# Performance work log

Measured on AMD Instinct MI355X. Metric: run time of the kernel, lower is better.

## Reference

```python
import jax, jax.numpy as jnp
import numpy as np

B, T, DIN, E, H, P = 8, 2048, 256, 256, 4, 8
HD = E // H


def _xavier(key, out_dim, in_dim):
    lim = float(np.sqrt(6.0 / (in_dim + out_dim)))
    return jax.random.uniform(key, (out_dim, in_dim), jnp.float32, -lim, lim)


def setup_inputs() -> dict:
    key = jax.random.key(0)
    ks = jax.random.split(key, 9)
    return {
        "x": jax.random.normal(ks[0], (B, T, DIN), jnp.float32),
        "w_in": _xavier(ks[1], E, DIN), "b_in": jnp.zeros((E,), jnp.float32),
        # MHA in-projections (torch packs qkv; xavier over packed [3E,E] approximated per-slice)
        "w_q": _xavier(ks[2], E, E), "b_q": jnp.zeros((E,), jnp.float32),
        "w_k": _xavier(ks[3], E, E), "b_k": jnp.zeros((E,), jnp.float32),
        "w_v": _xavier(ks[4], E, E), "b_v": jnp.zeros((E,), jnp.float32),
        "w_o": _xavier(ks[5], E, E), "b_o": jnp.zeros((E,), jnp.float32),
        "w_bd": _xavier(ks[6], 1, E), "b_bd": jnp.zeros((1,), jnp.float32),
        "w_pr": _xavier(ks[7], E, E), "b_pr": jnp.zeros((E,), jnp.float32),
    }


def reference(x, w_in, b_in, w_q, b_q, w_k, b_k, w_v, b_v, w_o, b_o, w_bd, b_bd, w_pr, b_pr):
    b, t, _ = x.shape
    h = x @ w_in.T + b_in                                   # [B,T,E]
    # self-attention (batch_first MHA, eval mode -> dropout is identity)
    q = (h @ w_q.T + b_q).reshape(b, t, H, HD)
    k = (h @ w_k.T + b_k).reshape(b, t, H, HD)
    v = (h @ w_v.T + b_v).reshape(b, t, H, HD)
    scale = 1.0 / np.sqrt(HD).astype(np.float32)
    scores = jnp.einsum("bqhd,bkhd->bhqk", q * scale, k)   # [B,H,T,T]
    attn = jax.nn.softmax(scores, axis=-1)
    ao = jnp.einsum("bhqk,bkhd->bqhd", attn, v).reshape(b, t, E)
    ao = ao @ w_o.T + b_o
    # boundary scoring -> dynamic patch ids
    bs = jax.nn.sigmoid(ao @ w_bd.T + b_bd)[..., 0]         # [B,T]
    cum = jnp.cumsum(bs, axis=1)
    normalized = cum / jnp.maximum(cum[:, -1:], 1e-6)
    pid = jnp.minimum((normalized * P).astype(jnp.int32), P - 1)  # [B,T]
    # mean-pool h into P dynamic patches (scatter_add + counts, via one-hot segment matmul)
    oh = jax.nn.one_hot(pid, P, dtype=h.dtype)              # [B,T,P]
    patch_emb = jnp.einsum("btp,btd->bpd", oh, h)           # [B,P,E]
    counts = oh.sum(axis=1)[..., None]                      # [B,P,1]
    patch_emb = patch_emb / jnp.maximum(counts, 1.0)
    return patch_emb @ w_pr.T + b_pr                        # [B,P,E]
```

## Files before the change

### kernel.cpp

```cpp
#include <hip/hip_runtime.h>
#include <cstddef>

#define NB 8
#define NT 2048
#define NE 256
#define NH 4
#define ND 64
#define NP 8

typedef short bf16x8 __attribute__((ext_vector_type(8)));
typedef float f32x4 __attribute__((ext_vector_type(4)));

__device__ __forceinline__ unsigned short f2bf(float f) {
  unsigned u = __builtin_bit_cast(unsigned, f);
  u += 0x7fffu + ((u >> 16) & 1u);
  return (unsigned short)(u >> 16);
}
__device__ __forceinline__ float bf2f(unsigned short h) {
  unsigned u = ((unsigned)h) << 16;
  return __builtin_bit_cast(float, u);
}
__device__ __forceinline__ void split2(float a, float b, unsigned& hi, unsigned& lo) {
  const unsigned short ha = f2bf(a), hb = f2bf(b);
  hi = (unsigned)ha | ((unsigned)hb << 16);
  const unsigned short la = f2bf(a - bf2f(ha));
  const unsigned short lb = f2bf(b - bf2f(hb));
  lo = (unsigned)la | ((unsigned)lb << 16);
}
__device__ __forceinline__ void gld16(const void* g, void* l) {
  __builtin_amdgcn_global_load_lds((const __attribute__((address_space(1))) unsigned*)g,
                                   (__attribute__((address_space(3))) unsigned*)l, 16, 0, 0);
}

#define QSC 0.180336880111120419f

__global__ __launch_bounds__(256) void setup_kernel(
    const float* __restrict__ w_in, const float* __restrict__ w_q,
    const float* __restrict__ w_k, const float* __restrict__ b_q,
    const float* __restrict__ b_k, const float* __restrict__ w_o,
    const float* __restrict__ b_o, const float* __restrict__ w_bd,
    const float* __restrict__ b_bd, const float* __restrict__ w_v,
    const float* __restrict__ b_v,
    unsigned short* __restrict__ wihi, unsigned short* __restrict__ wilo,
    unsigned short* __restrict__ wqkvhi, unsigned short* __restrict__ wqkvlo,
    float* __restrict__ bqk, float* __restrict__ consts, float* __restrict__ psum)
{
  __shared__ float wbd_s[NE];
  __shared__ float u_s[NE];
  const int b = blockIdx.x, tid = threadIdx.x;
  if (b < 512) {
    const int i = b * 256 + tid;
    const float v = (i < 65536) ? w_q[i] * QSC : w_k[i - 65536];
    const unsigned short h = f2bf(v);
    wqkvhi[i] = h;
    wqkvlo[i] = f2bf(v - bf2f(h));
    if (i < 512) bqk[i] = (i < 256) ? b_q[i] * QSC : b_k[i - 256];
  } else if (b < 576) {
    const int i = (b - 512) * 256 + tid;
    const float4 v = *(const float4*)(w_in + (size_t)i * 4);
    const float vv[4] = {v.x, v.y, v.z, v.w};
    unsigned short h4[4], l4[4];
    #pragma unroll
    for (int j = 0; j < 4; ++j) {
      h4[j] = f2bf(vv[j]);
      l4[j] = f2bf(vv[j] - bf2f(h4[j]));
    }
    *(ushort2*)(wihi + (size_t)i * 4)     = make_ushort2(h4[0], h4[1]);
    *(ushort2*)(wihi + (size_t)i * 4 + 2) = make_ushort2(h4[2], h4[3]);
    *(ushort2*)(wilo + (size_t)i * 4)     = make_ushort2(l4[0], l4[1]);
    *(ushort2*)(wilo + (size_t)i * 4 + 2) = make_ushort2(l4[2], l4[3]);
  } else if (b == 576) {
    wbd_s[tid] = w_bd[tid];
    __syncthreads();
    float a = 0.f;
    for (int j = 0; j < NE; ++j) a = fmaf(wbd_s[j], w_o[j * NE + tid], a);
    u_s[tid] = a;
    __syncthreads();
    #pragma unroll
    for (int hh = 0; hh < NH; ++hh) {
      float a2 = 0.f;
      for (int d = 0; d < ND; ++d)
        a2 = fmaf(u_s[hh * ND + d], w_v[(size_t)(hh * ND + d) * NE + tid], a2);
      const unsigned short hb = f2bf(a2);
      wqkvhi[(512 + hh) * 256 + tid] = hb;
      wqkvlo[(512 + hh) * 256 + tid] = f2bf(a2 - bf2f(hb));
    }
    for (int i = tid; i < 60 * 256; i += 256) {
      wqkvhi[516 * 256 + i] = 0;
      wqkvlo[516 * 256 + i] = 0;
    }
    if (tid == 0) {
      float cc = 0.f;
      for (int j = 0; j < NE; ++j) cc = fmaf(wbd_s[j], b_o[j], cc);
      consts[0] = cc + b_bd[0];
    }
    if (tid < 4) {
      float cv = 0.f;
      for (int d = 0; d < ND; ++d) cv = fmaf(u_s[tid * ND + d], b_v[tid * ND + d], cv);
      bqk[512 + tid] = cv;
    } else if (tid < 64) {
      bqk[512 + tid] = 0.f;
    }
  } else {
    for (int i = tid; i < NB * NP * NE; i += 256) psum[i] = 0.f;
  }
}

__global__ __launch_bounds__(256) void hgemm_kernel(
    const float* __restrict__ x,
    const unsigned short* __restrict__ wihi, const unsigned short* __restrict__ wilo,
    const float* __restrict__ b_in,
    unsigned short* __restrict__ hhi, unsigned short* __restrict__ hlo)
{
  __shared__ __align__(16) char sm[2][24576];
  const int tid = threadIdx.x;
  const int wave = tid >> 6, lane = tid & 63;
  const int lr = lane & 15, lg = lane >> 4;
  const int wm = wave >> 1, wn = wave & 1;
  const int bid = blockIdx.x;
  const int idx = bid >> 3;
  const int m0 = ((bid & 7) * 16 + (idx >> 2)) * 128;
  const int n0 = (idx & 3) * 64;

  const float* aSrc[4];
  #pragma unroll
  for (int c = 0; c < 4; ++c) {
    const int L = c * 4096 + tid * 16;
    const int row = L >> 7, w = (L >> 4) & 7;
    aSrc[c] = x + (size_t)(m0 + row) * 256 + (w ^ (row & 7)) * 4;
  }
  const unsigned short* wSrc[2];
  #pragma unroll
  for (int c = 0; c < 2; ++c) {
    const int L = c * 4096 + tid * 16;
    const int half = (L >> 12) & 1;
    const int Lh = L & 4095;
    const int col = Lh >> 6, w = (Lh >> 4) & 3;
    wSrc[c] = (half ? wilo : wihi) + (size_t)(n0 + col) * 256 + (w ^ ((col >> 1) & 3)) * 8;
  }
  int aoff[4][2], woff[2];
  #pragma unroll
  for (int s = 0; s < 4; ++s) {
    const int row = wm * 64 + s * 16 + lr;
    const int b0 = row * 128 + lg * 32;
    const int f = (row & 7) << 4;
    aoff[s][0] = b0 ^ f;
    aoff[s][1] = (b0 + 16) ^ f;
  }
  #pragma unroll
  for (int ns = 0; ns < 2; ++ns) {
    const int col = wn * 32 + ns * 16 + lr;
    woff[ns] = (col * 64 + lg * 16) ^ (((col >> 1) & 3) << 4);
  }

  f32x4 acc[4][2];
  #pragma unroll
  for (int s = 0; s < 4; ++s)
    #pragma unroll
    for (int ns = 0; ns < 2; ++ns) acc[s][ns] = (f32x4){0.f, 0.f, 0.f, 0.f};

  {
    char* lb = sm[0];
    #pragma unroll
    for (int c = 0; c < 4; ++c) gld16(aSrc[c], lb + c * 4096 + wave * 1024);
    #pragma unroll
    for (int c = 0; c < 2; ++c) gld16(wSrc[c], lb + 16384 + c * 4096 + wave * 1024);
  }

  for (int kt = 0; kt < 8; ++kt) {
    __syncthreads();
    if (kt < 7) {
      char* nb = sm[(kt + 1) & 1];
      #pragma unroll
      for (int c = 0; c < 4; ++c) gld16(aSrc[c] + (kt + 1) * 32, nb + c * 4096 + wave * 1024);
      #pragma unroll
      for (int c = 0; c < 2; ++c) gld16(wSrc[c] + (kt + 1) * 32, nb + 16384 + c * 4096 + wave * 1024);
    }
    const char* lb = sm[kt & 1];
    bf16x8 ah[4], al[4], wh[2], wl[2];
    #pragma unroll
    for (int s = 0; s < 4; ++s) {
      const f32x4 p0 = *(const f32x4*)(lb + aoff[s][0]);
      const f32x4 p1 = *(const f32x4*)(lb + aoff[s][1]);
      unsigned h0, h1, h2, h3, l0, l1, l2, l3;
      split2(p0[0], p0[1], h0, l0);
      split2(p0[2], p0[3], h1, l1);
      split2(p1[0], p1[1], h2, l2);
      split2(p1[2], p1[3], h3, l3);
      const uint4 hu = make_uint4(h0, h1, h2, h3);
      const uint4 lu = make_uint4(l0, l1, l2, l3);
      ah[s] = __builtin_bit_cast(bf16x8, hu);
      al[s] = __builtin_bit_cast(bf16x8, lu);
    }
    #pragma unroll
    for (int ns = 0; ns < 2; ++ns) {
      wh[ns] = *(const bf16x8*)(lb + 16384 + woff[ns]);
      wl[ns] = *(const bf16x8*)(lb + 20480 + woff[ns]);
    }
    #pragma unroll
    for (int s = 0; s < 4; ++s)
      #pragma unroll
      for (int ns = 0; ns < 2; ++ns) {
        acc[s][ns] = __builtin_amdgcn_mfma_f32_16x16x32_bf16(ah[s], wh[ns], acc[s][ns], 0, 0, 0);
        acc[s][ns] = __builtin_amdgcn_mfma_f32_16x16x32_bf16(ah[s], wl[ns], acc[s][ns], 0, 0, 0);
        acc[s][ns] = __builtin_amdgcn_mfma_f32_16x16x32_bf16(al[s], wh[ns], acc[s][ns], 0, 0, 0);
      }
  }
  #pragma unroll
  for (int s = 0; s < 4; ++s)
    #pragma unroll
    for (int ns = 0; ns < 2; ++ns)
      #pragma unroll
      for (int reg = 0; reg < 4; ++reg) {
        const int row = m0 + wm * 64 + s * 16 + lg * 4 + reg;
        const int col = n0 + wn * 32 + ns * 16 + lr;
        const float v = acc[s][ns][reg] + b_in[col];
        const size_t i2 = (size_t)row * 256 + col;
        const unsigned short hb = f2bf(v);
        hhi[i2] = hb;
        hlo[i2] = f2bf(v - bf2f(hb));
      }
}

__global__ __launch_bounds__(256) void qkvgemm_kernel(
    const unsigned short* __restrict__ Ahi, const unsigned short* __restrict__ Alo,
    const unsigned short* __restrict__ Whi, const unsigned short* __restrict__ Wlo,
    const float* __restrict__ bias,
    unsigned short* __restrict__ Qhi, unsigned short* __restrict__ Qlo,
    unsigned short* __restrict__ Khi, unsigned short* __restrict__ Klo,
    float* __restrict__ vubuf)
{
  __shared__ __align__(16) char sm[2][24576];
  const int tid = threadIdx.x;
  const int wave = tid >> 6, lane = tid & 63;
  const int lr = lane & 15, lg = lane >> 4;
  const int wm = wave >> 1, wn = wave & 1;
  const int bid = blockIdx.x;
  const int idx = bid >> 3;
  const int m0 = ((bid & 7) * 16 + idx / 9) * 128;
  const int n0 = (idx % 9) * 64;

  const unsigned short* aSrc[4];
  #pragma unroll
  for (int c = 0; c < 4; ++c) {
    const int L = c * 4096 + tid * 16;
    const int half = L >> 13;
    const int Lh = L & 8191;
    const int row = Lh >> 6, w = (Lh >> 4) & 3;
    aSrc[c] = (half ? Alo : Ahi) + (size_t)(m0 + row) * 256 + (w ^ ((row >> 1) & 3)) * 8;
  }
  const unsigned short* wSrc[2];
  #pragma unroll
  for (int c = 0; c < 2; ++c) {
    const int L = c * 4096 + tid * 16;
    const int half = (L >> 12) & 1;
    const int Lh = L & 4095;
    const int col = Lh >> 6, w = (Lh >> 4) & 3;
    wSrc[c] = (half ? Wlo : Whi) + (size_t)(n0 + col) * 256 + (w ^ ((col >> 1) & 3)) * 8;
  }
  int aoff[4], woff[2];
  #pragma unroll
  for (int s = 0; s < 4; ++s) {
    const int row = wm * 64 + s * 16 + lr;
    aoff[s] = (row * 64 + lg * 16) ^ (((row >> 1) & 3) << 4);
  }
  #pragma unroll
  for (int ns = 0; ns < 2; ++ns) {
    const int col = wn * 32 + ns * 16 + lr;
    woff[ns] = (col * 64 + lg * 16) ^ (((col >> 1) & 3) << 4);
  }

  f32x4 acc[4][2];
  #pragma unroll
  for (int s = 0; s < 4; ++s)
    #pragma unroll
    for (int ns = 0; ns < 2; ++ns) acc[s][ns] = (f32x4){0.f, 0.f, 0.f, 0.f};

  {
    char* lb = sm[0];
    #pragma unroll
    for (int c = 0; c < 4; ++c) gld16(aSrc[c], lb + c * 4096 + wave * 1024);
    #pragma unroll
    for (int c = 0; c < 2; ++c) gld16(wSrc[c], lb + 16384 + c * 4096 + wave * 1024);
  }

  for (int kt = 0; kt < 8; ++kt) {
    __syncthreads();
    if (kt < 7) {
      char* nb = sm[(kt + 1) & 1];
      #pragma unroll
      for (int c = 0; c < 4; ++c) gld16(aSrc[c] + (kt + 1) * 32, nb + c * 4096 + wave * 1024);
      #pragma unroll
      for (int c = 0; c < 2; ++c) gld16(wSrc[c] + (kt + 1) * 32, nb + 16384 + c * 4096 + wave * 1024);
    }
    const char* lb = sm[kt & 1];
    bf16x8 ah[4], al[4], wh[2], wl[2];
    #pragma unroll
    for (int s = 0; s < 4; ++s) {
      ah[s] = *(const bf16x8*)(lb + aoff[s]);
      al[s] = *(const bf16x8*)(lb + 8192 + aoff[s]);
    }
    #pragma unroll
    for (int ns = 0; ns < 2; ++ns) {
      wh[ns] = *(const bf16x8*)(lb + 16384 + woff[ns]);
      wl[ns] = *(const bf16x8*)(lb + 20480 + woff[ns]);
    }
    #pragma unroll
    for (int s = 0; s < 4; ++s)
      #pragma unroll
      for (int ns = 0; ns < 2; ++ns) {
        acc[s][ns] = __builtin_amdgcn_mfma_f32_16x16x32_bf16(ah[s], wh[ns], acc[s][ns], 0, 0, 0);
        acc[s][ns] = __builtin_amdgcn_mfma_f32_16x16x32_bf16(ah[s], wl[ns], acc[s][ns], 0, 0, 0);
        acc[s][ns] = __builtin_amdgcn_mfma_f32_16x16x32_bf16(al[s], wh[ns], acc[s][ns], 0, 0, 0);
      }
  }
  #pragma unroll
  for (int s = 0; s < 4; ++s)
    #pragma unroll
    for (int ns = 0; ns < 2; ++ns)
      #pragma unroll
      for (int reg = 0; reg < 4; ++reg) {
        const int row = m0 + wm * 64 + s * 16 + lg * 4 + reg;
        const int col = n0 + wn * 32 + ns * 16 + lr;
        const float v = acc[s][ns][reg] + bias[col];
        const int b = row >> 11, t = row & 2047;
        if (col < 512) {
          const int c = col & 255;
          const int head = c >> 6, d = c & 63;
          const size_t i2 = (((size_t)(b * NH + head)) * NT + t) * ND + d;
          const unsigned short hb = f2bf(v);
          if (col < 256) { Qhi[i2] = hb; Qlo[i2] = f2bf(v - bf2f(hb)); }
          else           { Khi[i2] = hb; Klo[i2] = f2bf(v - bf2f(hb)); }
        } else if (col < 516) {
          vubuf[((size_t)(b * NH + (col - 512))) * NT + t] = v;
        }
      }
}

__global__ __launch_bounds__(512) void attn_kernel8(
    const unsigned short* __restrict__ qhi, const unsigned short* __restrict__ qlo,
    const unsigned short* __restrict__ khi, const unsigned short* __restrict__ klo,
    const float* __restrict__ vu, float2* __restrict__ part2)
{
  __shared__ __align__(16) char kbuf[4][16384];
  __shared__ float vu_s[256];
  const int tid = threadIdx.x;
  const int wave = tid >> 6, lane = tid & 63;
  const int lr = lane & 15, lg = lane >> 4;
  const int bid = blockIdx.x;
  const int idx = bid >> 3;
  const int bh = (bid & 7) * 4 + (idx >> 6);
  const int rem = idx & 63;
  const int qt = rem >> 3, kh = rem & 7;
  const size_t base = (size_t)bh * NT * ND;
  const int qrow0 = qt * 256 + wave * 32;
  const int krow0 = kh * 256;

  if (tid < 256) vu_s[tid] = vu[(size_t)bh * NT + krow0 + tid];

  bf16x8 qf[2][2][2];
  #pragma unroll
  for (int s = 0; s < 2; ++s)
    #pragma unroll
    for (int ds = 0; ds < 2; ++ds) {
      const size_t off = base + (size_t)(qrow0 + s * 16 + lr) * ND + ds * 32 + lg * 8;
      qf[s][ds][0] = *(const bf16x8*)(qhi + off);
      qf[s][ds][1] = *(const bf16x8*)(qlo + off);
    }

  const int so = (tid * 16) ^ (((tid >> 3) & 7) << 4);
  int ro0[4], ro1[4];
  #pragma unroll
  for (int ns = 0; ns < 4; ++ns) {
    const int r = ns * 16 + lr;
    const int sw = (r & 7) << 4;
    const int ob = r * 128 + lg * 16;
    ro0[ns] = ob ^ sw;
    ro1[ns] = (ob + 64) ^ sw;
  }
  const char* srcH = (const char*)(khi + base + (size_t)krow0 * ND);
  const char* srcL = (const char*)(klo + base + (size_t)krow0 * ND);
  #pragma unroll
  for (int t = 0; t < 4; ++t) {
    gld16(srcH + t * 8192 + so, &kbuf[t][wave * 1024]);
    gld16(srcL + t * 8192 + so, &kbuf[t][8192 + wave * 1024]);
  }
  __syncthreads();

  float l[8], sv[8];
  #pragma unroll
  for (int i = 0; i < 8; ++i) { l[i] = 0.f; sv[i] = 0.f; }
  const f32x4 Z = (f32x4){0.f, 0.f, 0.f, 0.f};

  #pragma unroll
  for (int it = 0; it < 4; ++it) {
    const int kt = (it + wave) & 3;
    const char* kb = (const char*)kbuf[kt];
    f32x4 acc[2][4];
    float vuv[4];
    __builtin_amdgcn_s_setprio(1);
    #pragma unroll
    for (int ns = 0; ns < 4; ++ns) {
      const bf16x8 kh0 = *(const bf16x8*)(kb + ro0[ns]);
      const bf16x8 kh1 = *(const bf16x8*)(kb + ro1[ns]);
      const bf16x8 kl0 = *(const bf16x8*)(kb + 8192 + ro0[ns]);
      const bf16x8 kl1 = *(const bf16x8*)(kb + 8192 + ro1[ns]);
      vuv[ns] = vu_s[kt * 64 + ns * 16 + lr];
      #pragma unroll
      for (int s = 0; s < 2; ++s) {
        acc[s][ns] = __builtin_amdgcn_mfma_f32_16x16x32_bf16(qf[s][0][0], kh0, Z, 0, 0, 0);
        acc[s][ns] = __builtin_amdgcn_mfma_f32_16x16x32_bf16(qf[s][0][0], kl0, acc[s][ns], 0, 0, 0);
        acc[s][ns] = __builtin_amdgcn_mfma_f32_16x16x32_bf16(qf[s][0][1], kh0, acc[s][ns], 0, 0, 0);
        acc[s][ns] = __builtin_amdgcn_mfma_f32_16x16x32_bf16(qf[s][1][0], kh1, acc[s][ns], 0, 0, 0);
        acc[s][ns] = __builtin_amdgcn_mfma_f32_16x16x32_bf16(qf[s][1][0], kl1, acc[s][ns], 0, 0, 0);
        acc[s][ns] = __builtin_amdgcn_mfma_f32_16x16x32_bf16(qf[s][1][1], kh1, acc[s][ns], 0, 0, 0);
      }
    }
    __builtin_amdgcn_s_setprio(0);
    #pragma unroll
    for (int s = 0; s < 2; ++s)
      #pragma unroll
      for (int reg = 0; reg < 4; ++reg) {
        const int ri = s * 4 + reg;
        #pragma unroll
        for (int ns = 0; ns < 4; ++ns) {
          const float e = __builtin_amdgcn_exp2f(acc[s][ns][reg]);
          l[ri] += e;
          sv[ri] = fmaf(e, vuv[ns], sv[ri]);
        }
      }
  }
  #pragma unroll
  for (int ri = 0; ri < 8; ++ri) {
    #pragma unroll
    for (int off = 1; off < 16; off <<= 1) {
      l[ri]  += __shfl_xor(l[ri],  off, 16);
      sv[ri] += __shfl_xor(sv[ri], off, 16);
    }
  }
  if (lr == 0) {
    #pragma unroll
    for (int s = 0; s < 2; ++s)
      #pragma unroll
      for (int reg = 0; reg < 4; ++reg) {
        const int row = qrow0 + s * 16 + lg * 4 + reg;
        part2[(((size_t)bh * NT + row) << 3) + kh] = make_float2(l[s * 4 + reg], sv[s * 4 + reg]);
      }
  }
}

__global__ __launch_bounds__(256) void combine_kernel(
    const float4* __restrict__ part4, const float* __restrict__ consts,
    float* __restrict__ bs)
{
  const int gid = blockIdx.x * 256 + threadIdx.x;
  const int b = gid >> 11, t = gid & 2047;
  float logit = consts[0];
  #pragma unroll
  for (int hh = 0; hh < NH; ++hh) {
    const size_t p0 = ((size_t)((b * NH + hh) * NT) + t) * 4;
    float lsum = 0.f, ssum = 0.f;
    #pragma unroll
    for (int q = 0; q < 4; ++q) {
      const float4 p = part4[p0 + q];
      lsum += p.x + p.z;
      ssum += p.y + p.w;
    }
    logit += ssum / lsum;
  }
  bs[gid] = 1.f / (1.f + expf(-logit));
}

__global__ __launch_bounds__(256) void boundary_kernel(
    const float* __restrict__ bs, int* __restrict__ pid, int* __restrict__ counts)
{
  const int b = blockIdx.x, tid = threadIdx.x;
  __shared__ float partial[256];
  __shared__ int cnt_s[8];
  float v[8];
  float run = 0.f;
  const float4 b0 = *(const float4*)(bs + b * NT + tid * 8);
  const float4 b1 = *(const float4*)(bs + b * NT + tid * 8 + 4);
  const float bv[8] = {b0.x, b0.y, b0.z, b0.w, b1.x, b1.y, b1.z, b1.w};
  #pragma unroll
  for (int i = 0; i < 8; ++i) { run += bv[i]; v[i] = run; }
  float x = run;
  partial[tid] = x;
  __syncthreads();
  for (int off = 1; off < 256; off <<= 1) {
    const float y = (tid >= off) ? partial[tid - off] : 0.f;
    __syncthreads();
    x += y;
    partial[tid] = x;
    __syncthreads();
  }
  const float total = partial[255];
  if (tid < 8) cnt_s[tid] = 0;
  __syncthreads();
  const float denom = fmaxf(total, 1e-6f);
  const float excl = x - run;
  #pragma unroll
  for (int i = 0; i < 8; ++i) {
    const float norm = (excl + v[i]) / denom;
    int pp = (int)(norm * 8.f);
    pp = pp > 7 ? 7 : pp;
    pid[b * NT + tid * 8 + i] = pp;
    atomicAdd(&cnt_s[pp], 1);
  }
  __syncthreads();
  if (tid < 8) counts[b * 8 + tid] = cnt_s[tid];
}

__global__ __launch_bounds__(256) void pool_kernel(
    const unsigned short* __restrict__ hhi, const int* __restrict__ pid,
    float* __restrict__ psum)
{
  const int b = blockIdx.x >> 4, chunk = blockIdx.x & 15;
  const int tid = threadIdx.x;
  __shared__ int pid_s[128];
  const int t0 = chunk * 128;
  if (tid < 128) pid_s[tid] = pid[b * NT + t0 + tid];
  __syncthreads();
  float acc[8] = {};
  for (int tok = 0; tok < 128; ++tok) {
    const float val = bf2f(hhi[((size_t)b * NT + t0 + tok) * NE + tid]);
    const int p = pid_s[tok];
    #pragma unroll
    for (int pp = 0; pp < 8; ++pp) acc[pp] += (p == pp) ? val : 0.f;
  }
  #pragma unroll
  for (int pp = 0; pp < 8; ++pp)
    atomicAdd(&psum[((size_t)b * NP + pp) * NE + tid], acc[pp]);
}

__global__ __launch_bounds__(256) void final_kernel(
    const float* __restrict__ psum, const int* __restrict__ counts,
    const float* __restrict__ w_pr, const float* __restrict__ b_pr, float* __restrict__ out)
{
  const int bp = blockIdx.x;
  const int tid = threadIdx.x;
  __shared__ float pe[NE];
  const float cnt = fmaxf((float)counts[bp], 1.f);
  pe[tid] = psum[(size_t)bp * NE + tid] / cnt;
  __syncthreads();
  float acc = 0.f;
  for (int e = 0; e < NE; ++e) acc = fmaf(pe[e], w_pr[(size_t)tid * NE + e], acc);
  out[(size_t)bp * NE + tid] = acc + b_pr[tid];
}

extern "C" void kernel_launch(void* const* d_in, const int* in_sizes, int n_in,
                              void* d_out, int out_size, void* d_ws, size_t ws_size,
                              hipStream_t stream) {
  (void)in_sizes; (void)n_in; (void)out_size; (void)ws_size;
  const float* x    = (const float*)d_in[0];
  const float* w_in = (const float*)d_in[1];
  const float* b_in = (const float*)d_in[2];
  const float* w_q  = (const float*)d_in[3];
  const float* b_q  = (const float*)d_in[4];
  const float* w_k  = (const float*)d_in[5];
  const float* b_k  = (const float*)d_in[6];
  const float* w_v  = (const float*)d_in[7];
  const float* b_v  = (const float*)d_in[8];
  const float* w_o  = (const float*)d_in[9];
  const float* b_o  = (const float*)d_in[10];
  const float* w_bd = (const float*)d_in[11];
  const float* b_bd = (const float*)d_in[12];
  const float* w_pr = (const float*)d_in[13];
  const float* b_pr = (const float*)d_in[14];
  float* out = (float*)d_out;

  const size_t M = (size_t)NB * NT;
  unsigned short* hhi = (unsigned short*)d_ws;
  unsigned short* hlo = hhi + M * NE;
  unsigned short* qhi = hlo + M * NE;
  unsigned short* qlo = qhi + M * NE;
  unsigned short* khi = qlo + M * NE;
  unsigned short* klo = khi + M * NE;
  unsigned short* wihi = klo + M * NE;
  unsigned short* wilo = wihi + 65536;
  unsigned short* wqkvhi = wilo + 65536;
  unsigned short* wqkvlo = wqkvhi + 147456;
  float* bqk    = (float*)(wqkvlo + 147456);
  float* vubuf  = bqk + 576;
  float* part   = vubuf + 65536;
  float* bsbuf  = part + 1048576;
  float* consts = bsbuf + 16384;
  float* psum   = consts + 8;
  int*   pid    = (int*)(psum + 16384);
  int*   counts = pid + 16384;

  setup_kernel<<<578, 256, 0, stream>>>(w_in, w_q, w_k, b_q, b_k, w_o, b_o,
      w_bd, b_bd, w_v, b_v, wihi, wilo, wqkvhi, wqkvlo, bqk, consts, psum);
  hgemm_kernel<<<512, 256, 0, stream>>>(x, wihi, wilo, b_in, hhi, hlo);
  qkvgemm_kernel<<<1152, 256, 0, stream>>>(hhi, hlo, wqkvhi, wqkvlo, bqk,
      qhi, qlo, khi, klo, vubuf);
  attn_kernel8<<<2048, 512, 0, stream>>>(qhi, qlo, khi, klo, vubuf, (float2*)part);
  combine_kernel<<<64, 256, 0, stream>>>((const float4*)part, consts, bsbuf);
  boundary_kernel<<<8, 256, 0, stream>>>(bsbuf, pid, counts);
  pool_kernel<<<128, 256, 0, stream>>>(hhi, pid, psum);
  final_kernel<<<64, 256, 0, stream>>>(psum, counts, w_pr, b_pr, out);
}
```

Baseline: 154.1 us.

## Fold input projection into QKV weights and switch attention to 32x32 MFMA

Weights are precomposed on the device (w_q·w_in, w_k·w_in, and the v/boundary vector·w_in, with their biases folded in), so a single GEMM from x produces h, Q, K and the V-projection scalars. This removes the separate h GEMM pass and the hi/lo h round trip through memory. The attention kernel moves from 16x16x32 to 32x32x16 MFMA tiles with 16-row accumulators and adds an occupancy hint to launch bounds. The cost is an extra small setup kernel, a larger fused GEMM grid, and changed rounding from composing the weights before the bf16 split.

```diff
diff --git a/kernel.cpp b/kernel.cpp
--- a/kernel.cpp
+++ b/kernel.cpp
@@ -10,6 +10,7 @@
 
 typedef short bf16x8 __attribute__((ext_vector_type(8)));
 typedef float f32x4 __attribute__((ext_vector_type(4)));
+typedef float f32x16 __attribute__((ext_vector_type(16)));
 
 __device__ __forceinline__ unsigned short f2bf(float f) {
   unsigned u = __builtin_bit_cast(unsigned, f);
@@ -34,83 +35,93 @@
 
 #define QSC 0.180336880111120419f
 
-__global__ __launch_bounds__(256) void setup_kernel(
-    const float* __restrict__ w_in, const float* __restrict__ w_q,
-    const float* __restrict__ w_k, const float* __restrict__ b_q,
-    const float* __restrict__ b_k, const float* __restrict__ w_o,
-    const float* __restrict__ b_o, const float* __restrict__ w_bd,
-    const float* __restrict__ b_bd, const float* __restrict__ w_v,
-    const float* __restrict__ b_v,
-    unsigned short* __restrict__ wihi, unsigned short* __restrict__ wilo,
-    unsigned short* __restrict__ wqkvhi, unsigned short* __restrict__ wqkvlo,
-    float* __restrict__ bqk, float* __restrict__ consts, float* __restrict__ psum)
+__global__ __launch_bounds__(256) void setup1_kernel(
+    const float* __restrict__ w_o, const float* __restrict__ b_o,
+    const float* __restrict__ w_bd, const float* __restrict__ b_bd,
+    const float* __restrict__ w_v, const float* __restrict__ b_v,
+    float* __restrict__ uvbuf, float* __restrict__ consts)
 {
   __shared__ float wbd_s[NE];
   __shared__ float u_s[NE];
+  const int tid = threadIdx.x;
+  wbd_s[tid] = w_bd[tid];
+  __syncthreads();
+  float a = 0.f;
+  for (int j = 0; j < NE; ++j) a = fmaf(wbd_s[j], w_o[j * NE + tid], a);
+  u_s[tid] = a;
+  __syncthreads();
+  #pragma unroll
+  for (int hh = 0; hh < NH; ++hh) {
+    float a2 = 0.f;
+    for (int d = 0; d < ND; ++d)
+      a2 = fmaf(u_s[hh * ND + d], w_v[(size_t)(hh * ND + d) * NE + tid], a2);
+    uvbuf[hh * NE + tid] = a2;
+  }
+  if (tid == 0) {
+    float cc = 0.f;
+    for (int j = 0; j < NE; ++j) cc = fmaf(wbd_s[j], b_o[j], cc);
+    consts[0] = cc + b_bd[0];
+  }
+  if (tid >= 8 && tid < 12) {
+    const int hh = tid - 8;
+    float cv = 0.f;
+    for (int d = 0; d < ND; ++d) cv = fmaf(u_s[hh * ND + d], b_v[hh * ND + d], cv);
+    consts[1 + hh] = cv;
+  }
+}
+
+__global__ __launch_bounds__(256) void setup2_kernel(
+    const float* __restrict__ w_in, const float* __restrict__ w_q,
+    const float* __restrict__ w_k, const float* __restrict__ b_in,
+    const float* __restrict__ b_q, const float* __restrict__ b_k,
+    const float* __restrict__ uvbuf, const float* __restrict__ consts,
+    unsigned short* __restrict__ wfhi, unsigned short* __restrict__ wflo,
+    float* __restrict__ bias_f, float* __restrict__ psum)
+{
+  __shared__ float row_s[256];
+  __shared__ float red[256];
   const int b = blockIdx.x, tid = threadIdx.x;
-  if (b < 512) {
-    const int i = b * 256 + tid;
-    const float v = (i < 65536) ? w_q[i] * QSC : w_k[i - 65536];
-    const unsigned short h = f2bf(v);
-    wqkvhi[i] = h;
-    wqkvlo[i] = f2bf(v - bf2f(h));
-    if (i < 512) bqk[i] = (i < 256) ? b_q[i] * QSC : b_k[i - 256];
-  } else if (b < 576) {
-    const int i = (b - 512) * 256 + tid;
-    const float4 v = *(const float4*)(w_in + (size_t)i * 4);
-    const float vv[4] = {v.x, v.y, v.z, v.w};
-    unsigned short h4[4], l4[4];
-    #pragma unroll
-    for (int j = 0; j < 4; ++j) {
-      h4[j] = f2bf(vv[j]);
-      l4[j] = f2bf(vv[j] - bf2f(h4[j]));
-    }
-    *(ushort2*)(wihi + (size_t)i * 4)     = make_ushort2(h4[0], h4[1]);
-    *(ushort2*)(wihi + (size_t)i * 4 + 2) = make_ushort2(h4[2], h4[3]);
-    *(ushort2*)(wilo + (size_t)i * 4)     = make_ushort2(l4[0], l4[1]);
-    *(ushort2*)(wilo + (size_t)i * 4 + 2) = make_ushort2(l4[2], l4[3]);
-  } else if (b == 576) {
-    wbd_s[tid] = w_bd[tid];
+  if (b == 832) {
+    for (int i = tid; i < NB * NP * NE; i += 256) psum[i] = 0.f;
+    return;
+  }
+  float v = 0.f, bias = 0.f;
+  if (b < 256) {
+    v = w_in[(size_t)b * 256 + tid];
+    bias = b_in[b];
+  } else if (b < 772) {
+    const float* wrow = (b < 512) ? (w_q + (size_t)(b - 256) * 256)
+                      : (b < 768) ? (w_k + (size_t)(b - 512) * 256)
+                                  : (uvbuf + (size_t)(b - 768) * 256);
+    row_s[tid] = wrow[tid];
     __syncthreads();
-    float a = 0.f;
-    for (int j = 0; j < NE; ++j) a = fmaf(wbd_s[j], w_o[j * NE + tid], a);
-    u_s[tid] = a;
+    float acc = 0.f;
+    for (int e = 0; e < 256; ++e) acc = fmaf(row_s[e], w_in[(size_t)e * 256 + tid], acc);
+    v = acc;
+    red[tid] = row_s[tid] * b_in[tid];
     __syncthreads();
-    #pragma unroll
-    for (int hh = 0; hh < NH; ++hh) {
-      float a2 = 0.f;
-      for (int d = 0; d < ND; ++d)
-        a2 = fmaf(u_s[hh * ND + d], w_v[(size_t)(hh * ND + d) * NE + tid], a2);
-      const unsigned short hb = f2bf(a2);
-      wqkvhi[(512 + hh) * 256 + tid] = hb;
-      wqkvlo[(512 + hh) * 256 + tid] = f2bf(a2 - bf2f(hb));
-    }
-    for (int i = tid; i < 60 * 256; i += 256) {
-      wqkvhi[516 * 256 + i] = 0;
-      wqkvlo[516 * 256 + i] = 0;
-    }
-    if (tid == 0) {
-      float cc = 0.f;
-      for (int j = 0; j < NE; ++j) cc = fmaf(wbd_s[j], b_o[j], cc);
-      consts[0] = cc + b_bd[0];
-    }
-    if (tid < 4) {
-      float cv = 0.f;
-      for (int d = 0; d < ND; ++d) cv = fmaf(u_s[tid * ND + d], b_v[tid * ND + d], cv);
-      bqk[512 + tid] = cv;
-    } else if (tid < 64) {
-      bqk[512 + tid] = 0.f;
-    }
-  } else {
-    for (int i = tid; i < NB * NP * NE; i += 256) psum[i] = 0.f;
-  }
-}
-
-__global__ __launch_bounds__(256) void hgemm_kernel(
+    for (int off = 128; off > 0; off >>= 1) {
+      if (tid < off) red[tid] += red[tid + off];
+      __syncthreads();
+    }
+    bias = red[0] + ((b < 512) ? b_q[b - 256] : (b < 768) ? b_k[b - 512]
+                                              : consts[1 + (b - 768)]);
+    if (b < 512) { v *= QSC; bias *= QSC; }
+  }
+  const unsigned short hb = f2bf(v);
+  wfhi[(size_t)b * 256 + tid] = hb;
+  wflo[(size_t)b * 256 + tid] = f2bf(v - bf2f(hb));
+  if (tid == 0) bias_f[b] = bias;
+}
+
+__global__ __launch_bounds__(256) void xgemm_kernel(
     const float* __restrict__ x,
-    const unsigned short* __restrict__ wihi, const unsigned short* __restrict__ wilo,
-    const float* __restrict__ b_in,
-    unsigned short* __restrict__ hhi, unsigned short* __restrict__ hlo)
+    const unsigned short* __restrict__ wfhi, const unsigned short* __restrict__ wflo,
+    const float* __restrict__ bias_f,
+    unsigned short* __restrict__ hhi,
+    unsigned short* __restrict__ Qhi, unsigned short* __restrict__ Qlo,
+    unsigned short* __restrict__ Khi, unsigned short* __restrict__ Klo,
+    float* __restrict__ vubuf)
 {
   __shared__ __align__(16) char sm[2][24576];
   const int tid = threadIdx.x;
@@ -119,8 +130,8 @@
   const int wm = wave >> 1, wn = wave & 1;
   const int bid = blockIdx.x;
   const int idx = bid >> 3;
-  const int m0 = ((bid & 7) * 16 + (idx >> 2)) * 128;
-  const int n0 = (idx & 3) * 64;
+  const int m0 = ((bid & 7) * 16 + idx / 13) * 128;
+  const int n0 = (idx % 13) * 64;
 
   const float* aSrc[4];
   #pragma unroll
@@ -136,7 +147,7 @@
     const int half = (L >> 12) & 1;
     const int Lh = L & 4095;
     const int col = Lh >> 6, w = (Lh >> 4) & 3;
-    wSrc[c] = (half ? wilo : wihi) + (size_t)(n0 + col) * 256 + (w ^ ((col >> 1) & 3)) * 8;
+    wSrc[c] = (half ? wflo : wfhi) + (size_t)(n0 + col) * 256 + (w ^ ((col >> 1) & 3)) * 8;
   }
   int aoff[4][2], woff[2];
   #pragma unroll
@@ -214,130 +225,25 @@
       for (int reg = 0; reg < 4; ++reg) {
         const int row = m0 + wm * 64 + s * 16 + lg * 4 + reg;
         const int col = n0 + wn * 32 + ns * 16 + lr;
-        const float v = acc[s][ns][reg] + b_in[col];
-        const size_t i2 = (size_t)row * 256 + col;
-        const unsigned short hb = f2bf(v);
-        hhi[i2] = hb;
-        hlo[i2] = f2bf(v - bf2f(hb));
-      }
-}
-
-__global__ __launch_bounds__(256) void qkvgemm_kernel(
-    const unsigned short* __restrict__ Ahi, const unsigned short* __restrict__ Alo,
-    const unsigned short* __restrict__ Whi, const unsigned short* __restrict__ Wlo,
-    const float* __restrict__ bias,
-    unsigned short* __restrict__ Qhi, unsigned short* __restrict__ Qlo,
-    unsigned short* __restrict__ Khi, unsigned short* __restrict__ Klo,
-    float* __restrict__ vubuf)
-{
-  __shared__ __align__(16) char sm[2][24576];
-  const int tid = threadIdx.x;
-  const int wave = tid >> 6, lane = tid & 63;
-  const int lr = lane & 15, lg = lane >> 4;
-  const int wm = wave >> 1, wn = wave & 1;
-  const int bid = blockIdx.x;
-  const int idx = bid >> 3;
-  const int m0 = ((bid & 7) * 16 + idx / 9) * 128;
-  const int n0 = (idx % 9) * 64;
-
-  const unsigned short* aSrc[4];
-  #pragma unroll
-  for (int c = 0; c < 4; ++c) {
-    const int L = c * 4096 + tid * 16;
-    const int half = L >> 13;
-    const int Lh = L & 8191;
-    const int row = Lh >> 6, w = (Lh >> 4) & 3;
-    aSrc[c] = (half ? Alo : Ahi) + (size_t)(m0 + row) * 256 + (w ^ ((row >> 1) & 3)) * 8;
-  }
-  const unsigned short* wSrc[2];
-  #pragma unroll
-  for (int c = 0; c < 2; ++c) {
-    const int L = c * 4096 + tid * 16;
-    const int half = (L >> 12) & 1;
-    const int Lh = L & 4095;
-    const int col = Lh >> 6, w = (Lh >> 4) & 3;
-    wSrc[c] = (half ? Wlo : Whi) + (size_t)(n0 + col) * 256 + (w ^ ((col >> 1) & 3)) * 8;
-  }
-  int aoff[4], woff[2];
-  #pragma unroll
-  for (int s = 0; s < 4; ++s) {
-    const int row = wm * 64 + s * 16 + lr;
-    aoff[s] = (row * 64 + lg * 16) ^ (((row >> 1) & 3) << 4);
-  }
-  #pragma unroll
-  for (int ns = 0; ns < 2; ++ns) {
-    const int col = wn * 32 + ns * 16 + lr;
-    woff[ns] = (col * 64 + lg * 16) ^ (((col >> 1) & 3) << 4);
-  }
-
-  f32x4 acc[4][2];
-  #pragma unroll
-  for (int s = 0; s < 4; ++s)
-    #pragma unroll
-    for (int ns = 0; ns < 2; ++ns) acc[s][ns] = (f32x4){0.f, 0.f, 0.f, 0.f};
-
-  {
-    char* lb = sm[0];
-    #pragma unroll
-    for (int c = 0; c < 4; ++c) gld16(aSrc[c], lb + c * 4096 + wave * 1024);
-    #pragma unroll
-    for (int c = 0; c < 2; ++c) gld16(wSrc[c], lb + 16384 + c * 4096 + wave * 1024);
-  }
-
-  for (int kt = 0; kt < 8; ++kt) {
-    __syncthreads();
-    if (kt < 7) {
-      char* nb = sm[(kt + 1) & 1];
-      #pragma unroll
-      for (int c = 0; c < 4; ++c) gld16(aSrc[c] + (kt + 1) * 32, nb + c * 4096 + wave * 1024);
-      #pragma unroll
-      for (int c = 0; c < 2; ++c) gld16(wSrc[c] + (kt + 1) * 32, nb + 16384 + c * 4096 + wave * 1024);
-    }
-    const char* lb = sm[kt & 1];
-    bf16x8 ah[4], al[4], wh[2], wl[2];
-    #pragma unroll
-    for (int s = 0; s < 4; ++s) {
-      ah[s] = *(const bf16x8*)(lb + aoff[s]);
-      al[s] = *(const bf16x8*)(lb + 8192 + aoff[s]);
-    }
-    #pragma unroll
-    for (int ns = 0; ns < 2; ++ns) {
-      wh[ns] = *(const bf16x8*)(lb + 16384 + woff[ns]);
-      wl[ns] = *(const bf16x8*)(lb + 20480 + woff[ns]);
-    }
-    #pragma unroll
-    for (int s = 0; s < 4; ++s)
-      #pragma unroll
-      for (int ns = 0; ns < 2; ++ns) {
-        acc[s][ns] = __builtin_amdgcn_mfma_f32_16x16x32_bf16(ah[s], wh[ns], acc[s][ns], 0, 0, 0);
-        acc[s][ns] = __builtin_amdgcn_mfma_f32_16x16x32_bf16(ah[s], wl[ns], acc[s][ns], 0, 0, 0);
-        acc[s][ns] = __builtin_amdgcn_mfma_f32_16x16x32_bf16(al[s], wh[ns], acc[s][ns], 0, 0, 0);
-      }
-  }
-  #pragma unroll
-  for (int s = 0; s < 4; ++s)
-    #pragma unroll
-    for (int ns = 0; ns < 2; ++ns)
-      #pragma unroll
-      for (int reg = 0; reg < 4; ++reg) {
-        const int row = m0 + wm * 64 + s * 16 + lg * 4 + reg;
-        const int col = n0 + wn * 32 + ns * 16 + lr;
-        const float v = acc[s][ns][reg] + bias[col];
+        const float v = acc[s][ns][reg] + bias_f[col];
         const int b = row >> 11, t = row & 2047;
-        if (col < 512) {
-          const int c = col & 255;
+        if (col < 256) {
+          hhi[(size_t)row * 256 + col] = f2bf(v);
+        } else if (col < 768) {
+          const int c = (col - 256) & 255;
           const int head = c >> 6, d = c & 63;
           const size_t i2 = (((size_t)(b * NH + head)) * NT + t) * ND + d;
           const unsigned short hb = f2bf(v);
-          if (col < 256) { Qhi[i2] = hb; Qlo[i2] = f2bf(v - bf2f(hb)); }
-          else           { Khi[i2] = hb; Klo[i2] = f2bf(v - bf2f(hb)); }
-        } else if (col < 516) {
-          vubuf[((size_t)(b * NH + (col - 512))) * NT + t] = v;
+          const unsigned short lb2 = f2bf(v - bf2f(hb));
+          if (col < 512) { Qhi[i2] = hb; Qlo[i2] = lb2; }
+          else           { Khi[i2] = hb; Klo[i2] = lb2; }
+        } else if (col < 772) {
+          vubuf[((size_t)(b * NH + (col - 768))) * NT + t] = v;
         }
       }
 }
 
-__global__ __launch_bounds__(512) void attn_kernel8(
+__global__ __launch_bounds__(512, 4) void attn_kernel9(
     const unsigned short* __restrict__ qhi, const unsigned short* __restrict__ qlo,
     const unsigned short* __restrict__ khi, const unsigned short* __restrict__ klo,
     const float* __restrict__ vu, float2* __restrict__ part2)
@@ -346,7 +252,8 @@
   __shared__ float vu_s[256];
   const int tid = threadIdx.x;
   const int wave = tid >> 6, lane = tid & 63;
-  const int lr = lane & 15, lg = lane >> 4;
+  const int lk = lane & 31;
+  const int lh = lane >> 5;
   const int bid = blockIdx.x;
   const int idx = bid >> 3;
   const int bh = (bid & 7) * 4 + (idx >> 6);
@@ -358,26 +265,22 @@
 
   if (tid < 256) vu_s[tid] = vu[(size_t)bh * NT + krow0 + tid];
 
-  bf16x8 qf[2][2][2];
-  #pragma unroll
-  for (int s = 0; s < 2; ++s)
-    #pragma unroll
-    for (int ds = 0; ds < 2; ++ds) {
-      const size_t off = base + (size_t)(qrow0 + s * 16 + lr) * ND + ds * 32 + lg * 8;
-      qf[s][ds][0] = *(const bf16x8*)(qhi + off);
-      qf[s][ds][1] = *(const bf16x8*)(qlo + off);
-    }
+  bf16x8 qf[4][2];
+  #pragma unroll
+  for (int ds = 0; ds < 4; ++ds) {
+    const size_t off = base + (size_t)(qrow0 + lk) * ND + ds * 16 + lh * 8;
+    qf[ds][0] = *(const bf16x8*)(qhi + off);
+    qf[ds][1] = *(const bf16x8*)(qlo + off);
+  }
 
   const int so = (tid * 16) ^ (((tid >> 3) & 7) << 4);
-  int ro0[4], ro1[4];
-  #pragma unroll
-  for (int ns = 0; ns < 4; ++ns) {
-    const int r = ns * 16 + lr;
-    const int sw = (r & 7) << 4;
-    const int ob = r * 128 + lg * 16;
-    ro0[ns] = ob ^ sw;
-    ro1[ns] = (ob + 64) ^ sw;
-  }
+  int ro[2][4];
+  #pragma unroll
+  for (int sub = 0; sub < 2; ++sub)
+    #pragma unroll
+    for (int ds = 0; ds < 4; ++ds)
+      ro[sub][ds] = (sub * 32 + lk) * 128 + ((32 * ds + 16 * lh) ^ ((lk & 7) << 4));
+
   const char* srcH = (const char*)(khi + base + (size_t)krow0 * ND);
   const char* srcL = (const char*)(klo + base + (size_t)krow0 * ND);
   #pragma unroll
@@ -387,65 +290,73 @@
   }
   __syncthreads();
 
-  float l[8], sv[8];
-  #pragma unroll
-  for (int i = 0; i < 8; ++i) { l[i] = 0.f; sv[i] = 0.f; }
-  const f32x4 Z = (f32x4){0.f, 0.f, 0.f, 0.f};
+  float l[16], sv[16];
+  #pragma unroll
+  for (int i = 0; i < 16; ++i) { l[i] = 0.f; sv[i] = 0.f; }
+  f32x16 Z;
+  #pragma unroll
+  for (int i = 0; i < 16; ++i) Z[i] = 0.f;
 
   #pragma unroll
   for (int it = 0; it < 4; ++it) {
     const int kt = (it + wave) & 3;
     const char* kb = (const char*)kbuf[kt];
-    f32x4 acc[2][4];
-    float vuv[4];
-    __builtin_amdgcn_s_setprio(1);
-    #pragma unroll
-    for (int ns = 0; ns < 4; ++ns) {
-      const bf16x8 kh0 = *(const bf16x8*)(kb + ro0[ns]);
-      const bf16x8 kh1 = *(const bf16x8*)(kb + ro1[ns]);
-      const bf16x8 kl0 = *(const bf16x8*)(kb + 8192 + ro0[ns]);
-      const bf16x8 kl1 = *(const bf16x8*)(kb + 8192 + ro1[ns]);
-      vuv[ns] = vu_s[kt * 64 + ns * 16 + lr];
+    #pragma unroll
+    for (int sub = 0; sub < 2; ++sub) {
+      const float vuv = vu_s[kt * 64 + sub * 32 + lk];
+      f32x16 acc;
+      __builtin_amdgcn_s_setprio(1);
+      {
+        const bf16x8 kh0 = *(const bf16x8*)(kb + ro[sub][0]);
+        const bf16x8 kl0 = *(const bf16x8*)(kb + 8192 + ro[sub][0]);
+        acc = __builtin_amdgcn_mfma_f32_32x32x16_bf16(qf[0][0], kh0, Z, 0, 0, 0);
+        acc = __builtin_amdgcn_mfma_f32_32x32x16_bf16(qf[0][0], kl0, acc, 0, 0, 0);
+        acc = __builtin_amdgcn_mfma_f32_32x32x16_bf16(qf[0][1], kh0, acc, 0, 0, 0);
+      }
+      {
+        const bf16x8 kh1 = *(const bf16x8*)(kb + ro[sub][1]);
+        const bf16x8 kl1 = *(const bf16x8*)(kb + 8192 + ro[sub][1]);
+        acc = __builtin_amdgcn_mfma_f32_32x32x16_bf16(qf[1][0], kh1, acc, 0, 0, 0);
+        acc = __builtin_amdgcn_mfma_f32_32x32x16_bf16(qf[1][0], kl1, acc, 0, 0, 0);
+        acc = __builtin_amdgcn_mfma_f32_32x32x16_bf16(qf[1][1], kh1, acc, 0, 0, 0);
+      }
+      {
+        const bf16x8 kh2 = *(const bf16x8*)(kb + ro[sub][2]);
+        const bf16x8 kl2 = *(const bf16x8*)(kb + 8192 + ro[sub][2]);
+        acc = __builtin_amdgcn_mfma_f32_32x32x16_bf16(qf[2][0], kh2, acc, 0, 0, 0);
+        acc = __builtin_amdgcn_mfma_f32_32x32x16_bf16(qf[2][0], kl2, acc, 0, 0, 0);
+        acc = __builtin_amdgcn_mfma_f32_32x32x16_bf16(qf[2][1], kh2, acc, 0, 0, 0);
+      }
+      {
+        const bf16x8 kh3 = *(const bf16x8*)(kb + ro[sub][3]);
+        const bf16x8 kl3 = *(const bf16x8*)(kb + 8192 + ro[sub][3]);
+        acc = __builtin_amdgcn_mfma_f32_32x32x16_bf16(qf[3][0], kh3, acc, 0, 0, 0);
+        acc = __builtin_amdgcn_mfma_f32_32x32x16_bf16(qf[3][0], kl3, acc, 0, 0, 0);
+        acc = __builtin_amdgcn_mfma_f32_32x32x16_bf16(qf[3][1], kh3, acc, 0, 0, 0);
+      }
+      __builtin_amdgcn_s_setprio(0);
       #pragma unroll
-      for (int s = 0; s < 2; ++s) {
-        acc[s][ns] = __builtin_amdgcn_mfma_f32_16x16x32_bf16(qf[s][0][0], kh0, Z, 0, 0, 0);
-        acc[s][ns] = __builtin_amdgcn_mfma_f32_16x16x32_bf16(qf[s][0][0], kl0, acc[s][ns], 0, 0, 0);
-        acc[s][ns] = __builtin_amdgcn_mfma_f32_16x16x32_bf16(qf[s][0][1], kh0, acc[s][ns], 0, 0, 0);
-        acc[s][ns] = __builtin_amdgcn_mfma_f32_16x16x32_bf16(qf[s][1][0], kh1, acc[s][ns], 0, 0, 0);
-        acc[s][ns] = __builtin_amdgcn_mfma_f32_16x16x32_bf16(qf[s][1][0], kl1, acc[s][ns], 0, 0, 0);
-        acc[s][ns] = __builtin_amdgcn_mfma_f32_16x16x32_bf16(qf[s][1][1], kh1, acc[s][ns], 0, 0, 0);
-      }
-    }
-    __builtin_amdgcn_s_setprio(0);
-    #pragma unroll
-    for (int s = 0; s < 2; ++s)
-      #pragma unroll
-      for (int reg = 0; reg < 4; ++reg) {
-        const int ri = s * 4 + reg;
-        #pragma unroll
-        for (int ns = 0; ns < 4; ++ns) {
-          const float e = __builtin_amdgcn_exp2f(acc[s][ns][reg]);
-          l[ri] += e;
-          sv[ri] = fmaf(e, vuv[ns], sv[ri]);
-        }
-      }
-  }
-  #pragma unroll
-  for (int ri = 0; ri < 8; ++ri) {
-    #pragma unroll
-    for (int off = 1; off < 16; off <<= 1) {
-      l[ri]  += __shfl_xor(l[ri],  off, 16);
-      sv[ri] += __shfl_xor(sv[ri], off, 16);
-    }
-  }
-  if (lr == 0) {
-    #pragma unroll
-    for (int s = 0; s < 2; ++s)
-      #pragma unroll
-      for (int reg = 0; reg < 4; ++reg) {
-        const int row = qrow0 + s * 16 + lg * 4 + reg;
-        part2[(((size_t)bh * NT + row) << 3) + kh] = make_float2(l[s * 4 + reg], sv[s * 4 + reg]);
-      }
+      for (int reg = 0; reg < 16; ++reg) {
+        const float e = __builtin_amdgcn_exp2f(acc[reg]);
+        l[reg] += e;
+        sv[reg] = fmaf(e, vuv, sv[reg]);
+      }
+    }
+  }
+  #pragma unroll
+  for (int reg = 0; reg < 16; ++reg) {
+    #pragma unroll
+    for (int off = 1; off < 32; off <<= 1) {
+      l[reg]  += __shfl_xor(l[reg],  off);
+      sv[reg] += __shfl_xor(sv[reg], off);
+    }
+  }
+  if (lk == 0) {
+    #pragma unroll
+    for (int reg = 0; reg < 16; ++reg) {
+      const int row = qrow0 + (reg & 3) + 8 * (reg >> 2) + 4 * lh;
+      part2[(((size_t)bh * NT + row) << 3) + kh] = make_float2(l[reg], sv[reg]);
+    }
   }
 }
 
@@ -571,17 +482,15 @@
 
   const size_t M = (size_t)NB * NT;
   unsigned short* hhi = (unsigned short*)d_ws;
-  unsigned short* hlo = hhi + M * NE;
-  unsigned short* qhi = hlo + M * NE;
+  unsigned short* qhi = hhi + M * NE;
   unsigned short* qlo = qhi + M * NE;
   unsigned short* khi = qlo + M * NE;
   unsigned short* klo = khi + M * NE;
-  unsigned short* wihi = klo + M * NE;
-  unsigned short* wilo = wihi + 65536;
-  unsigned short* wqkvhi = wilo + 65536;
-  unsigned short* wqkvlo = wqkvhi + 147456;
-  float* bqk    = (float*)(wqkvlo + 147456);
-  float* vubuf  = bqk + 576;
+  unsigned short* wfhi = klo + M * NE;
+  unsigned short* wflo = wfhi + 212992;
+  float* bias_f = (float*)(wflo + 212992);
+  float* uvbuf  = bias_f + 832;
+  float* vubuf  = uvbuf + 1024;
   float* part   = vubuf + 65536;
   float* bsbuf  = part + 1048576;
   float* consts = bsbuf + 16384;
@@ -589,12 +498,12 @@
   int*   pid    = (int*)(psum + 16384);
   int*   counts = pid + 16384;
 
-  setup_kernel<<<578, 256, 0, stream>>>(w_in, w_q, w_k, b_q, b_k, w_o, b_o,
-      w_bd, b_bd, w_v, b_v, wihi, wilo, wqkvhi, wqkvlo, bqk, consts, psum);
-  hgemm_kernel<<<512, 256, 0, stream>>>(x, wihi, wilo, b_in, hhi, hlo);
-  qkvgemm_kernel<<<1152, 256, 0, stream>>>(hhi, hlo, wqkvhi, wqkvlo, bqk,
-      qhi, qlo, khi, klo, vubuf);
-  attn_kernel8<<<2048, 512, 0, stream>>>(qhi, qlo, khi, klo, vubuf, (float2*)part);
+  setup1_kernel<<<1, 256, 0, stream>>>(w_o, b_o, w_bd, b_bd, w_v, b_v, uvbuf, consts);
+  setup2_kernel<<<833, 256, 0, stream>>>(w_in, w_q, w_k, b_in, b_q, b_k,
+      uvbuf, consts, wfhi, wflo, bias_f, psum);
+  xgemm_kernel<<<1664, 256, 0, stream>>>(x, wfhi, wflo, bias_f,
+      hhi, qhi, qlo, khi, klo, vubuf);
+  attn_kernel9<<<2048, 512, 0, stream>>>(qhi, qlo, khi, klo, vubuf, (float2*)part);
   combine_kernel<<<64, 256, 0, stream>>>((const float4*)part, consts, bsbuf);
   boundary_kernel<<<8, 256, 0, stream>>>(bsbuf, pid, counts);
   pool_kernel<<<128, 256, 0, stream>>>(hhi, pid, psum);
```

Measured after the change: 181.2 us. 1.18x slower.
